# Kernel tuning notes

Hardware: AMD Instinct MI355X
Metric: run time of the kernel (lower is better)

## Reference

```python
import jax, jax.numpy as jnp
import numpy as np

N = 20000
E = 320000
D_IN = 1024
D_OUT = 1024


def setup_inputs() -> dict:
    key = jax.random.key(0)
    k1, k2, k3, k4 = jax.random.split(key, 4)
    x = jax.random.normal(k1, (N, D_IN), dtype=jnp.float32)
    edge_index = jax.random.randint(k2, (2, E), 0, N, dtype=jnp.int64)
    # nn.Linear params: W is [out, in], b is [out]
    W = jax.random.normal(k3, (D_OUT, D_IN), dtype=jnp.float32) * (1.0 / np.sqrt(D_IN))
    b = jax.random.normal(k4, (D_OUT,), dtype=jnp.float32) * 0.01
    return {"x": x, "edge_index": edge_index, "W": W, "b": b}


def reference(x, edge_index, W, b):
    num_nodes = x.shape[0]
    # add self-connections (same as addSelfConnect)
    self_idx = jnp.arange(num_nodes, dtype=edge_index.dtype)
    ei = jnp.concatenate([edge_index, jnp.stack([self_idx, self_idx], axis=0)], axis=1)
    row, col = ei[0], ei[1]
    # linear: h = x @ W^T + b  -> [N, D_OUT]
    h = jnp.einsum('nd,od->no', x, W) + b
    # degree computed from row indices only (matches calDegree(row, ...))
    deg = jnp.zeros((num_nodes,), dtype=h.dtype).at[row].add(1.0)
    deg_inv_sqrt = deg ** -0.5  # every node has a self-loop, so deg >= 1
    norm = deg_inv_sqrt[row] * deg_inv_sqrt[col]  # [E+N]
    # gather source features, scale per-edge, scatter-sum to destination nodes
    msg = norm[:, None] * h[col]  # [E+N, D_OUT]
    out = jax.ops.segment_sum(msg, row, num_segments=num_nodes)
    return out
```

## Files before the change

kernel.cpp:

```cpp
#include <hip/hip_runtime.h>
#include <hip/hip_bf16.h>
#include <stdint.h>
#include <stddef.h>


#define D_DIM 1024

typedef __bf16 bf16x8 __attribute__((ext_vector_type(8)));
typedef __bf16 bf16x4 __attribute__((ext_vector_type(4)));
typedef float  f32x4  __attribute__((ext_vector_type(4)));

#define GLOBAL_AS __attribute__((address_space(1)))
#define LDS_AS    __attribute__((address_space(3)))

static __device__ __forceinline__ void async_load16(const void* g, void* l) {
  __builtin_amdgcn_global_load_lds((GLOBAL_AS void*)(void*)g,
                                   (LDS_AS void*)l, 16, 0, 0);
}


__global__ void detect_kernel(const unsigned int* __restrict__ xw,
                              const unsigned int* __restrict__ ww,
                              const unsigned int* __restrict__ ew,
                              int* __restrict__ flags) {
  __shared__ int s[3];
  int t = threadIdx.x;
  if (t < 3) s[t] = 0;
  __syncthreads();
  int nx = 0, nw = 0, ze = 0;
  for (int i = t; i < 8192; i += 256) {
    if ((xw[i] & 0x7f80u) == 0x7f80u) nx++;
    if ((ww[i] & 0x7f80u) == 0x7f80u) nw++;
    if (ew[2 * i + 1] == 0u) ze++;
  }
  atomicAdd(&s[0], nx);
  atomicAdd(&s[1], nw);
  atomicAdd(&s[2], ze);
  __syncthreads();
  if (t == 0) {
    flags[0] = (s[0] >= 3) ? 1 : 0;
    flags[1] = (s[1] >= 3) ? 1 : 0;
    flags[2] = (s[2] >= 8000) ? 1 : 0;
  }
}


__global__ void zero_cnt_kernel(int* cnt, int n) {
  int i = blockIdx.x * blockDim.x + threadIdx.x;
  if (i < n) cnt[i] = 0;
}

__global__ void count_deg_kernel(const void* __restrict__ ei, int E,
                                 const int* __restrict__ flags,
                                 int* __restrict__ cnt) {
  int e = blockIdx.x * blockDim.x + threadIdx.x;
  if (e < E) {
    int r = flags[2] ? (int)((const long long*)ei)[e] : ((const int*)ei)[e];
    atomicAdd(&cnt[r], 1);
  }
}

__global__ void scan_kernel(const int* __restrict__ cnt, int n,
                            int* __restrict__ row_ptr, int* __restrict__ cursor,
                            float* __restrict__ dinv) {
  __shared__ int ssum[256];
  const int t = threadIdx.x;
  const int chunk = (n + 255) / 256;
  const int lo = t * chunk;
  const int hi = (lo + chunk < n) ? lo + chunk : n;
  int s = 0;
  for (int i = lo; i < hi; ++i) s += cnt[i];
  ssum[t] = s;
  __syncthreads();
  for (int off = 1; off < 256; off <<= 1) {
    int add = (t >= off) ? ssum[t - off] : 0;
    __syncthreads();
    ssum[t] += add;
    __syncthreads();
  }
  int run = ssum[t] - s;
  for (int i = lo; i < hi; ++i) {
    int v = cnt[i];
    row_ptr[i] = run;
    cursor[i]  = run;
    dinv[i] = rsqrtf((float)(v + 1));
    run += v;
  }
  if (t == 255) row_ptr[n] = ssum[255];
}

__global__ void scatter_kernel(const void* __restrict__ ei, int E,
                               const int* __restrict__ flags,
                               const float* __restrict__ dinv,
                               int* __restrict__ cursor,
                               int* __restrict__ cols_out,
                               float* __restrict__ wgt, int emit_w) {
  int e = blockIdx.x * blockDim.x + threadIdx.x;
  if (e < E) {
    int r, c;
    if (flags[2]) {
      const long long* p = (const long long*)ei;
      r = (int)p[e]; c = (int)p[e + E];
    } else {
      const int* p = (const int*)ei;
      r = p[e]; c = p[e + E];
    }
    int pos = atomicAdd(&cursor[r], 1);
    cols_out[pos] = c;
    if (emit_w) wgt[pos] = dinv[r] * dinv[c];
  }
}


__global__ void conv_w_kernel(const void* __restrict__ W,
                              const void* __restrict__ b,
                              const int* __restrict__ flags,
                              unsigned short* __restrict__ Wb,
                              float* __restrict__ biasf) {
  int i = blockIdx.x * blockDim.x + threadIdx.x;
  int wfp = flags[1];
  if (wfp) {
    __bf16 h = (__bf16)((const float*)W)[i];
    Wb[i] = *(unsigned short*)&h;
  } else {
    Wb[i] = ((const unsigned short*)W)[i];
  }
  if (i < D_DIM) {
    biasf[i] = wfp ? ((const float*)b)[i] : (float)((const __bf16*)b)[i];
  }
}


__global__ __launch_bounds__(256) void conv_x_kernel(
    const void* __restrict__ X, const int* __restrict__ flags,
    unsigned short* __restrict__ Xb, int total8) {
  int i = blockIdx.x * blockDim.x + threadIdx.x;
  if (i >= total8) return;
  if (!flags[0]) return;
  const float* p = (const float*)X + (size_t)i * 8;
  f32x4 v0 = *(const f32x4*)p;
  f32x4 v1 = *(const f32x4*)(p + 4);
  bf16x8 r;
  r[0] = (__bf16)v0[0]; r[1] = (__bf16)v0[1];
  r[2] = (__bf16)v0[2]; r[3] = (__bf16)v0[3];
  r[4] = (__bf16)v1[0]; r[5] = (__bf16)v1[1];
  r[6] = (__bf16)v1[2]; r[7] = (__bf16)v1[3];
  *(bf16x8*)(Xb + (size_t)i * 8) = r;
}


__global__ __launch_bounds__(256) void gemm_xw2_kernel(
    const void* __restrict__ Xv,
    const unsigned short* __restrict__ Xb,
    const unsigned short* __restrict__ Wb,
    const float* __restrict__ biasf,
    const int* __restrict__ flags,
    __hip_bfloat16* __restrict__ H,
    int M) {
  __shared__ unsigned short As[128 * 32];
  __shared__ unsigned short Bs[128 * 32];

  const int t    = threadIdx.x;
  const int lane = t & 63;
  const int wave = t >> 6;
  const int wm   = wave >> 1;
  const int wn   = wave & 1;

  const int nwg = gridDim.x;
  const int wg  = (blockIdx.x & 7) * (nwg >> 3) + (blockIdx.x >> 3);
  const int m0  = (wg >> 3) * 128;
  const int n0  = (wg & 7) * 128;

  const unsigned short* Asrc =
      flags[0] ? Xb : (const unsigned short*)Xv;

  f32x4 acc[4][4] = {};

  const int ra = t >> 2;
  const int kc = (t & 3) * 8;
  int gr0 = m0 + ra;       if (gr0 >= M) gr0 = M - 1;
  int gr1 = m0 + 64 + ra;  if (gr1 >= M) gr1 = M - 1;
  const int quad = lane >> 4;
  const int mrow = lane & 15;

  for (int k0 = 0; k0 < D_DIM; k0 += 32) {
    async_load16(Asrc + (size_t)gr0 * D_DIM + k0 + kc, &As[ra * 32 + kc]);
    async_load16(Asrc + (size_t)gr1 * D_DIM + k0 + kc, &As[(ra + 64) * 32 + kc]);
    async_load16(Wb + (size_t)(n0 + ra) * D_DIM + k0 + kc, &Bs[ra * 32 + kc]);
    async_load16(Wb + (size_t)(n0 + ra + 64) * D_DIM + k0 + kc,
                 &Bs[(ra + 64) * 32 + kc]);
    __syncthreads();

    bf16x8 a[4], b[4];
#pragma unroll
    for (int i = 0; i < 4; ++i)
      a[i] = *(const bf16x8*)&As[(wm * 64 + i * 16 + mrow) * 32 + quad * 8];
#pragma unroll
    for (int j = 0; j < 4; ++j)
      b[j] = *(const bf16x8*)&Bs[(wn * 64 + j * 16 + mrow) * 32 + quad * 8];
#pragma unroll
    for (int i = 0; i < 4; ++i)
#pragma unroll
      for (int j = 0; j < 4; ++j)
        acc[i][j] = __builtin_amdgcn_mfma_f32_16x16x32_bf16(a[i], b[j], acc[i][j], 0, 0, 0);
    __syncthreads();
  }

#pragma unroll
  for (int j = 0; j < 4; ++j) {
    int n = n0 + wn * 64 + j * 16 + mrow;
    float bn = biasf[n];
#pragma unroll
    for (int i = 0; i < 4; ++i) {
      int mb = m0 + wm * 64 + i * 16 + quad * 4;
#pragma unroll
      for (int rg = 0; rg < 4; ++rg) {
        int m = mb + rg;
        if (m < M) H[(size_t)m * D_DIM + n] = __float2bfloat16(acc[i][j][rg] + bn);
      }
    }
  }
}


__global__ __launch_bounds__(256) void gemm_xw_kernel(
    const void* __restrict__ Xv,
    const unsigned short* __restrict__ Wb,
    const float* __restrict__ biasf,
    const int* __restrict__ flags,
    __hip_bfloat16* __restrict__ H,
    int M) {
  __shared__ unsigned short As[128 * 32];
  __shared__ unsigned short Bs[128 * 32];

  const int t    = threadIdx.x;
  const int lane = t & 63;
  const int wave = t >> 6;
  const int wm   = wave >> 1;
  const int wn   = wave & 1;
  const int m0   = blockIdx.x * 128;
  const int n0   = blockIdx.y * 128;
  const int xfp  = flags[0];

  f32x4 acc[4][4] = {};

  const int ra = t >> 1;
  const int kh = (t & 1) * 16;
  const int rb = t >> 2;
  const int kc = (t & 3) * 8;
  const int quad = lane >> 4;
  const int mrow = lane & 15;

  for (int k0 = 0; k0 < D_DIM; k0 += 32) {
    async_load16(Wb + (size_t)(n0 + rb) * D_DIM + k0 + kc, &Bs[rb * 32 + kc]);
    async_load16(Wb + (size_t)(n0 + rb + 64) * D_DIM + k0 + kc,
                 &Bs[(rb + 64) * 32 + kc]);
    bf16x8 lo{}, hi{};
    int gm = m0 + ra;
    if (gm < M) {
      if (xfp) {
        const float* p = (const float*)Xv + (size_t)gm * D_DIM + k0 + kh;
        f32x4 v0 = *(const f32x4*)(p);
        f32x4 v1 = *(const f32x4*)(p + 4);
        f32x4 v2 = *(const f32x4*)(p + 8);
        f32x4 v3 = *(const f32x4*)(p + 12);
        lo[0] = (__bf16)v0[0]; lo[1] = (__bf16)v0[1];
        lo[2] = (__bf16)v0[2]; lo[3] = (__bf16)v0[3];
        lo[4] = (__bf16)v1[0]; lo[5] = (__bf16)v1[1];
        lo[6] = (__bf16)v1[2]; lo[7] = (__bf16)v1[3];
        hi[0] = (__bf16)v2[0]; hi[1] = (__bf16)v2[1];
        hi[2] = (__bf16)v2[2]; hi[3] = (__bf16)v2[3];
        hi[4] = (__bf16)v3[0]; hi[5] = (__bf16)v3[1];
        hi[6] = (__bf16)v3[2]; hi[7] = (__bf16)v3[3];
      } else {
        const unsigned short* p =
            (const unsigned short*)Xv + (size_t)gm * D_DIM + k0 + kh;
        lo = *(const bf16x8*)p;
        hi = *(const bf16x8*)(p + 8);
      }
    }
    *(bf16x8*)&As[ra * 32 + kh]     = lo;
    *(bf16x8*)&As[ra * 32 + kh + 8] = hi;
    __syncthreads();

    bf16x8 a[4], b[4];
#pragma unroll
    for (int i = 0; i < 4; ++i)
      a[i] = *(const bf16x8*)&As[(wm * 64 + i * 16 + mrow) * 32 + quad * 8];
#pragma unroll
    for (int j = 0; j < 4; ++j)
      b[j] = *(const bf16x8*)&Bs[(wn * 64 + j * 16 + mrow) * 32 + quad * 8];
#pragma unroll
    for (int i = 0; i < 4; ++i)
#pragma unroll
      for (int j = 0; j < 4; ++j)
        acc[i][j] = __builtin_amdgcn_mfma_f32_16x16x32_bf16(a[i], b[j], acc[i][j], 0, 0, 0);
    __syncthreads();
  }

#pragma unroll
  for (int j = 0; j < 4; ++j) {
    int n = n0 + wn * 64 + j * 16 + mrow;
    float bn = biasf[n];
#pragma unroll
    for (int i = 0; i < 4; ++i) {
      int mb = m0 + wm * 64 + i * 16 + quad * 4;
#pragma unroll
      for (int rg = 0; rg < 4; ++rg) {
        int m = mb + rg;
        if (m < M) H[(size_t)m * D_DIM + n] = __float2bfloat16(acc[i][j][rg] + bn);
      }
    }
  }
}


__global__ __launch_bounds__(256) void aggregate_h_kernel(
    const __hip_bfloat16* __restrict__ H,
    const int* __restrict__ row_ptr,
    const int* __restrict__ cols,
    const float* __restrict__ wgt,
    const float* __restrict__ dinv,
    const int* __restrict__ flags,
    void* __restrict__ outv, int M) {
  const int lane = threadIdx.x & 63;
  const int i = blockIdx.x * 4 + (threadIdx.x >> 6);
  if (i >= M) return;
  const int c0 = lane * 16;

  float a[16];
  {
    float di = dinv[i];
    float w = di * di;
    const __hip_bfloat16* p = H + (size_t)i * D_DIM + c0;
    bf16x8 v0 = *(const bf16x8*)p;
    bf16x8 v1 = *(const bf16x8*)(p + 8);
#pragma unroll
    for (int k = 0; k < 8; ++k) {
      a[k]     = w * (float)v0[k];
      a[8 + k] = w * (float)v1[k];
    }
  }
  const int e0 = row_ptr[i], e1 = row_ptr[i + 1];
  for (int e = e0; e < e1; ++e) {
    int c = cols[e];
    float w = wgt[e];
    const __hip_bfloat16* p = H + (size_t)c * D_DIM + c0;
    bf16x8 u0 = *(const bf16x8*)p;
    bf16x8 u1 = *(const bf16x8*)(p + 8);
#pragma unroll
    for (int k = 0; k < 8; ++k) {
      a[k]     += w * (float)u0[k];
      a[8 + k] += w * (float)u1[k];
    }
  }
  if (flags[0]) {
    float* o = (float*)outv + (size_t)i * D_DIM + c0;
#pragma unroll
    for (int q = 0; q < 4; ++q) {
      f32x4 r; r[0] = a[4*q]; r[1] = a[4*q+1]; r[2] = a[4*q+2]; r[3] = a[4*q+3];
      *(f32x4*)(o + 4 * q) = r;
    }
  } else {
    __hip_bfloat16* o = (__hip_bfloat16*)outv + (size_t)i * D_DIM + c0;
    bf16x8 r0, r1;
#pragma unroll
    for (int k = 0; k < 8; ++k) { r0[k] = (__bf16)a[k]; r1[k] = (__bf16)a[8+k]; }
    *(bf16x8*)o = r0;
    *(bf16x8*)(o + 8) = r1;
  }
}


__global__ __launch_bounds__(256) void aggregate_x_kernel(
    const void* __restrict__ X,
    const int* __restrict__ row_ptr,
    const int* __restrict__ cols,
    const float* __restrict__ dinv,
    const int* __restrict__ flags,
    float* __restrict__ rowsum,
    void* __restrict__ Y) {
  const int i  = blockIdx.x;
  const int c0 = threadIdx.x * 4;
  const float di = dinv[i];
  const int e0 = row_ptr[i], e1 = row_ptr[i + 1];
  float wsum = di * di;
  float a0, a1, a2, a3;

  if (flags[0]) {
    const float* Xf = (const float*)X;
    f32x4 v = *(const f32x4*)(Xf + (size_t)i * D_DIM + c0);
    a0 = wsum * v[0]; a1 = wsum * v[1]; a2 = wsum * v[2]; a3 = wsum * v[3];
    for (int e = e0; e < e1; ++e) {
      int c = cols[e];
      float w = di * dinv[c];
      wsum += w;
      f32x4 u = *(const f32x4*)(Xf + (size_t)c * D_DIM + c0);
      a0 += w * u[0]; a1 += w * u[1]; a2 += w * u[2]; a3 += w * u[3];
    }
    f32x4 r; r[0] = a0; r[1] = a1; r[2] = a2; r[3] = a3;
    *(f32x4*)((float*)Y + (size_t)i * D_DIM + c0) = r;
  } else {
    const __hip_bfloat16* Xb = (const __hip_bfloat16*)X;
    bf16x4 v = *(const bf16x4*)(Xb + (size_t)i * D_DIM + c0);
    a0 = wsum * (float)v[0]; a1 = wsum * (float)v[1];
    a2 = wsum * (float)v[2]; a3 = wsum * (float)v[3];
    for (int e = e0; e < e1; ++e) {
      int c = cols[e];
      float w = di * dinv[c];
      wsum += w;
      bf16x4 u = *(const bf16x4*)(Xb + (size_t)c * D_DIM + c0);
      a0 += w * (float)u[0]; a1 += w * (float)u[1];
      a2 += w * (float)u[2]; a3 += w * (float)u[3];
    }
    bf16x4 r;
    r[0] = (__bf16)a0; r[1] = (__bf16)a1; r[2] = (__bf16)a2; r[3] = (__bf16)a3;
    *(bf16x4*)((__hip_bfloat16*)Y + (size_t)i * D_DIM + c0) = r;
  }
  if (threadIdx.x == 0) rowsum[i] = wsum;
}

__global__ __launch_bounds__(256) void strip_gemm_kernel(
    const void* __restrict__ Yv,
    const unsigned short* __restrict__ Wb,
    const float* __restrict__ biasf,
    const float* __restrict__ rowsum,
    const int* __restrict__ flags,
    void* __restrict__ outv) {
  __shared__ unsigned short Ys[32 * 1024];

  const int t    = threadIdx.x;
  const int lane = t & 63;
  const int wave = t >> 6;
  const int m0   = blockIdx.x * 32;
  const int ofp  = flags[0];

  if (ofp) {
    const float* Yf = (const float*)Yv;
    for (int idx = t; idx < 32 * 128; idx += 256) {
      int r = idx >> 7, c = idx & 127;
      const float* p = Yf + (size_t)(m0 + r) * D_DIM + c * 8;
      f32x4 lo = *(const f32x4*)p;
      f32x4 hi = *(const f32x4*)(p + 4);
      bf16x8 v;
      v[0] = (__bf16)lo[0]; v[1] = (__bf16)lo[1];
      v[2] = (__bf16)lo[2]; v[3] = (__bf16)lo[3];
      v[4] = (__bf16)hi[0]; v[5] = (__bf16)hi[1];
      v[6] = (__bf16)hi[2]; v[7] = (__bf16)hi[3];
      int sc = c ^ (r & 15);
      *(bf16x8*)&Ys[r * 1024 + sc * 8] = v;
    }
  } else {
    const __hip_bfloat16* Yb = (const __hip_bfloat16*)Yv;
    for (int idx = t; idx < 32 * 128; idx += 256) {
      int r = idx >> 7, c = idx & 127;
      bf16x8 v = *(const bf16x8*)(Yb + (size_t)(m0 + r) * D_DIM + c * 8);
      int sc = c ^ (r & 15);
      *(bf16x8*)&Ys[r * 1024 + sc * 8] = v;
    }
  }
  __syncthreads();

  const int quad = lane >> 4;
  const int mrow = lane & 15;

  for (int nb = 0; nb < 4; ++nb) {
    f32x4 acc[2][4] = {};
    for (int k0 = 0; k0 < D_DIM; k0 += 32) {
      const int cbase = k0 >> 3;
      bf16x8 a[2], b[4];
#pragma unroll
      for (int i = 0; i < 2; ++i) {
        int m = i * 16 + mrow;
        int sc = (cbase + quad) ^ mrow;
        a[i] = *(const bf16x8*)&Ys[m * 1024 + sc * 8];
      }
#pragma unroll
      for (int j = 0; j < 4; ++j) {
        int n = wave * 256 + nb * 64 + j * 16 + mrow;
        b[j] = *(const bf16x8*)(Wb + (size_t)n * D_DIM + k0 + quad * 8);
      }
#pragma unroll
      for (int i = 0; i < 2; ++i)
#pragma unroll
        for (int j = 0; j < 4; ++j)
          acc[i][j] = __builtin_amdgcn_mfma_f32_16x16x32_bf16(a[i], b[j], acc[i][j], 0, 0, 0);
    }
#pragma unroll
    for (int j = 0; j < 4; ++j) {
      int n = wave * 256 + nb * 64 + j * 16 + mrow;
      float bn = biasf[n];
#pragma unroll
      for (int i = 0; i < 2; ++i) {
        int mb = m0 + i * 16 + quad * 4;
#pragma unroll
        for (int rg = 0; rg < 4; ++rg) {
          int m = mb + rg;
          float val = acc[i][j][rg] + rowsum[m] * bn;
          if (ofp) ((float*)outv)[(size_t)m * D_DIM + n] = val;
          else ((__hip_bfloat16*)outv)[(size_t)m * D_DIM + n] = __float2bfloat16(val);
        }
      }
    }
  }
}


extern "C" void kernel_launch(void* const* d_in, const int* in_sizes, int n_in,
                              void* d_out, int out_size, void* d_ws, size_t ws_size,
                              hipStream_t stream) {
  const void* x    = d_in[0];
  const void* ei   = d_in[1];
  const void* Wm   = d_in[2];
  const void* bias = d_in[3];

  const int E = in_sizes[1] / 2;
  const int M = in_sizes[0] / D_DIM;

  char* ws = (char*)d_ws;
  const size_t KB = 1024, MB = 1024 * 1024;

  const size_t szH = (size_t)M * D_DIM * 2;
  const size_t need_fast   = 6 * MB + szH + MB;
  const size_t need_faster = 6 * MB + 2 * szH + MB;

  if (ws_size >= need_fast) {
    int*   flags   = (int*)(ws);
    int*   cnt     = (int*)(ws + 4 * KB);
    int*   row_ptr = (int*)(ws + 128 * KB);
    int*   cursor  = (int*)(ws + 256 * KB);
    float* dinv    = (float*)(ws + 384 * KB);
    float* biasf   = (float*)(ws + 512 * KB);
    int*   cols    = (int*)(ws + 768 * KB);
    float* wgt     = (float*)(ws + 2 * MB);
    unsigned short* Wb = (unsigned short*)(ws + 4 * MB);
    __hip_bfloat16* H  = (__hip_bfloat16*)(ws + 6 * MB);
    unsigned short* Xb = (unsigned short*)(ws + 6 * MB + szH);

    detect_kernel<<<1, 256, 0, stream>>>((const unsigned int*)x,
                                         (const unsigned int*)Wm,
                                         (const unsigned int*)ei, (int*)flags);
    zero_cnt_kernel<<<(M + 255) / 256, 256, 0, stream>>>(cnt, M);
    count_deg_kernel<<<(E + 255) / 256, 256, 0, stream>>>(ei, E, flags, cnt);
    scan_kernel<<<1, 256, 0, stream>>>(cnt, M, row_ptr, cursor, dinv);
    scatter_kernel<<<(E + 255) / 256, 256, 0, stream>>>(ei, E, flags, dinv,
                                                        cursor, cols, wgt, 1);
    conv_w_kernel<<<(D_DIM * D_DIM) / 256, 256, 0, stream>>>(Wm, bias, flags,
                                                             Wb, biasf);
    const int mtiles = (M + 127) / 128;
    if (ws_size >= need_faster) {
      const int total8 = M * (D_DIM / 8);
      conv_x_kernel<<<(total8 + 255) / 256, 256, 0, stream>>>(x, flags, Xb,
                                                              total8);
      gemm_xw2_kernel<<<mtiles * 8, 256, 0, stream>>>(x, Xb, Wb, biasf, flags,
                                                      H, M);
    } else {
      dim3 ggrid(mtiles, D_DIM / 128);
      gemm_xw_kernel<<<ggrid, 256, 0, stream>>>(x, Wb, biasf, flags, H, M);
    }
    aggregate_h_kernel<<<(M + 3) / 4, 256, 0, stream>>>(H, row_ptr, cols, wgt,
                                                        dinv, flags, d_out, M);
  } else {
    int*   flags   = (int*)(ws);
    int*   cnt     = (int*)(ws + 4 * KB);
    int*   row_ptr = (int*)(ws + 128 * KB);
    int*   cursor  = (int*)(ws + 256 * KB);
    float* dinv    = (float*)(ws + 384 * KB);
    float* rowsum  = (float*)(ws + 512 * KB);
    float* biasf   = (float*)(ws + 640 * KB);
    int*   cols    = (int*)(ws + 768 * KB);
    unsigned short* Wb = (unsigned short*)(ws + 2 * MB);

    detect_kernel<<<1, 256, 0, stream>>>((const unsigned int*)x,
                                         (const unsigned int*)Wm,
                                         (const unsigned int*)ei, (int*)flags);
    zero_cnt_kernel<<<(M + 255) / 256, 256, 0, stream>>>(cnt, M);
    count_deg_kernel<<<(E + 255) / 256, 256, 0, stream>>>(ei, E, flags, cnt);
    scan_kernel<<<1, 256, 0, stream>>>(cnt, M, row_ptr, cursor, dinv);
    scatter_kernel<<<(E + 255) / 256, 256, 0, stream>>>(ei, E, flags, dinv,
                                                        cursor, cols, (float*)0, 0);
    conv_w_kernel<<<(D_DIM * D_DIM) / 256, 256, 0, stream>>>(Wm, bias, flags,
                                                             Wb, biasf);
    aggregate_x_kernel<<<M, 256, 0, stream>>>(x, row_ptr, cols, dinv, flags,
                                              rowsum, d_out);
    strip_gemm_kernel<<<M / 32, 256, 0, stream>>>(d_out, Wb, biasf, rowsum,
                                                  flags, d_out);
  }
}
```

Before: 428.3 us.

## Slab-tile aggregation over feature columns with padded H and packed edge metadata

The aggregation kernel now splits the 1024 feature columns into 16 slabs of 64 and assigns 8 threads per node per slab. Slab-major block ordering keeps the gathered working set of H small enough to stay cache-resident while all nodes are processed. H rows are padded to 1088 elements to avoid channel or bank aliasing. Column index and edge weight are packed into one 64-bit word, the edge loop is unrolled by four with FMAs, and outputs use nontemporal stores. The cost is 16 times more row_ptr and metadata reads, extra workspace for the padding, and a possible stride-related change in GEMM write efficiency.

```diff
diff --git a/kernel.cpp b/kernel.cpp
--- a/kernel.cpp
+++ b/kernel.cpp
@@ -5,6 +5,10 @@
 
 
 #define D_DIM 1024
+#define HP    1088
+#define HPB   2176u
+#define SLABW 64
+#define NSLAB (D_DIM / SLABW)
 
 typedef __bf16 bf16x8 __attribute__((ext_vector_type(8)));
 typedef __bf16 bf16x4 __attribute__((ext_vector_type(4)));
@@ -94,7 +98,7 @@
                                const float* __restrict__ dinv,
                                int* __restrict__ cursor,
                                int* __restrict__ cols_out,
-                               float* __restrict__ wgt, int emit_w) {
+                               long long* __restrict__ meta, int emit_w) {
   int e = blockIdx.x * blockDim.x + threadIdx.x;
   if (e < E) {
     int r, c;
@@ -106,8 +110,14 @@
       r = p[e]; c = p[e + E];
     }
     int pos = atomicAdd(&cursor[r], 1);
-    cols_out[pos] = c;
-    if (emit_w) wgt[pos] = dinv[r] * dinv[c];
+    if (emit_w) {
+      float w = dinv[r] * dinv[c];
+      unsigned long long mm =
+          ((unsigned long long)__float_as_uint(w) << 32) | (unsigned)c;
+      meta[pos] = (long long)mm;
+    } else {
+      cols_out[pos] = c;
+    }
   }
 }
 
@@ -216,7 +226,7 @@
 #pragma unroll
       for (int rg = 0; rg < 4; ++rg) {
         int m = mb + rg;
-        if (m < M) H[(size_t)m * D_DIM + n] = __float2bfloat16(acc[i][j][rg] + bn);
+        if (m < M) H[(size_t)m * HP + n] = __float2bfloat16(acc[i][j][rg] + bn);
       }
     }
   }
@@ -308,66 +318,88 @@
 #pragma unroll
       for (int rg = 0; rg < 4; ++rg) {
         int m = mb + rg;
-        if (m < M) H[(size_t)m * D_DIM + n] = __float2bfloat16(acc[i][j][rg] + bn);
+        if (m < M) H[(size_t)m * HP + n] = __float2bfloat16(acc[i][j][rg] + bn);
       }
     }
   }
 }
 
 
-__global__ __launch_bounds__(256) void aggregate_h_kernel(
+__global__ __launch_bounds__(256) void aggregate_h_slab_kernel(
     const __hip_bfloat16* __restrict__ H,
     const int* __restrict__ row_ptr,
-    const int* __restrict__ cols,
-    const float* __restrict__ wgt,
+    const long long* __restrict__ meta,
     const float* __restrict__ dinv,
     const int* __restrict__ flags,
-    void* __restrict__ outv, int M) {
-  const int lane = threadIdx.x & 63;
-  const int i = blockIdx.x * 4 + (threadIdx.x >> 6);
+    void* __restrict__ outv, int M, int nodeblks) {
+  const int slab = blockIdx.x / nodeblks;
+  const int nb   = blockIdx.x - slab * nodeblks;
+  const int t    = threadIdx.x;
+  const int i    = nb * 32 + (t >> 3);
   if (i >= M) return;
-  const int c0 = lane * 16;
-
-  float a[16];
+  const int l = t & 7;
+  const unsigned co = (unsigned)l * 16u;
+  const char* Hs = (const char*)H + (unsigned)slab * 128u;
+
+  float a[8];
   {
     float di = dinv[i];
     float w = di * di;
-    const __hip_bfloat16* p = H + (size_t)i * D_DIM + c0;
-    bf16x8 v0 = *(const bf16x8*)p;
-    bf16x8 v1 = *(const bf16x8*)(p + 8);
-#pragma unroll
-    for (int k = 0; k < 8; ++k) {
-      a[k]     = w * (float)v0[k];
-      a[8 + k] = w * (float)v1[k];
-    }
-  }
+    bf16x8 v = *(const bf16x8*)(Hs + (unsigned)i * HPB + co);
+#pragma unroll
+    for (int k = 0; k < 8; ++k) a[k] = w * (float)v[k];
+  }
+
   const int e0 = row_ptr[i], e1 = row_ptr[i + 1];
-  for (int e = e0; e < e1; ++e) {
-    int c = cols[e];
-    float w = wgt[e];
-    const __hip_bfloat16* p = H + (size_t)c * D_DIM + c0;
-    bf16x8 u0 = *(const bf16x8*)p;
-    bf16x8 u1 = *(const bf16x8*)(p + 8);
-#pragma unroll
-    for (int k = 0; k < 8; ++k) {
-      a[k]     += w * (float)u0[k];
-      a[8 + k] += w * (float)u1[k];
-    }
-  }
+  int e = e0;
+  for (; e + 4 <= e1; e += 4) {
+    long long m0 = meta[e];
+    long long m1 = meta[e + 1];
+    long long m2 = meta[e + 2];
+    long long m3 = meta[e + 3];
+    unsigned o0 = (unsigned)(m0 & 0xffffffffLL) * HPB + co;
+    unsigned o1 = (unsigned)(m1 & 0xffffffffLL) * HPB + co;
+    unsigned o2 = (unsigned)(m2 & 0xffffffffLL) * HPB + co;
+    unsigned o3 = (unsigned)(m3 & 0xffffffffLL) * HPB + co;
+    float w0 = __uint_as_float((unsigned)((unsigned long long)m0 >> 32));
+    float w1 = __uint_as_float((unsigned)((unsigned long long)m1 >> 32));
+    float w2 = __uint_as_float((unsigned)((unsigned long long)m2 >> 32));
+    float w3 = __uint_as_float((unsigned)((unsigned long long)m3 >> 32));
+    bf16x8 u0 = *(const bf16x8*)(Hs + o0);
+    bf16x8 u1 = *(const bf16x8*)(Hs + o1);
+    bf16x8 u2 = *(const bf16x8*)(Hs + o2);
+    bf16x8 u3 = *(const bf16x8*)(Hs + o3);
+#pragma unroll
+    for (int q = 0; q < 8; ++q) {
+      a[q] = fmaf(w0, (float)u0[q],
+             fmaf(w1, (float)u1[q],
+             fmaf(w2, (float)u2[q],
+             fmaf(w3, (float)u3[q], a[q]))));
+    }
+  }
+  for (; e < e1; ++e) {
+    long long m0 = meta[e];
+    unsigned o0 = (unsigned)(m0 & 0xffffffffLL) * HPB + co;
+    float w0 = __uint_as_float((unsigned)((unsigned long long)m0 >> 32));
+    bf16x8 u0 = *(const bf16x8*)(Hs + o0);
+#pragma unroll
+    for (int q = 0; q < 8; ++q) a[q] = fmaf(w0, (float)u0[q], a[q]);
+  }
+
   if (flags[0]) {
-    float* o = (float*)outv + (size_t)i * D_DIM + c0;
-#pragma unroll
-    for (int q = 0; q < 4; ++q) {
-      f32x4 r; r[0] = a[4*q]; r[1] = a[4*q+1]; r[2] = a[4*q+2]; r[3] = a[4*q+3];
-      *(f32x4*)(o + 4 * q) = r;
-    }
+    float* o = (float*)outv + (size_t)i * D_DIM + slab * SLABW + l * 8;
+    f32x4 r0, r1;
+    r0[0] = a[0]; r0[1] = a[1]; r0[2] = a[2]; r0[3] = a[3];
+    r1[0] = a[4]; r1[1] = a[5]; r1[2] = a[6]; r1[3] = a[7];
+    __builtin_nontemporal_store(r0, (f32x4*)o);
+    __builtin_nontemporal_store(r1, (f32x4*)(o + 4));
   } else {
-    __hip_bfloat16* o = (__hip_bfloat16*)outv + (size_t)i * D_DIM + c0;
-    bf16x8 r0, r1;
-#pragma unroll
-    for (int k = 0; k < 8; ++k) { r0[k] = (__bf16)a[k]; r1[k] = (__bf16)a[8+k]; }
-    *(bf16x8*)o = r0;
-    *(bf16x8*)(o + 8) = r1;
+    __hip_bfloat16* o =
+        (__hip_bfloat16*)outv + (size_t)i * D_DIM + slab * SLABW + l * 8;
+    bf16x8 r;
+#pragma unroll
+    for (int k = 0; k < 8; ++k) r[k] = (__bf16)a[k];
+    __builtin_nontemporal_store(*(f32x4*)&r, (f32x4*)o);
   }
 }
 
@@ -520,22 +552,34 @@
   char* ws = (char*)d_ws;
   const size_t KB = 1024, MB = 1024 * 1024;
 
-  const size_t szH = (size_t)M * D_DIM * 2;
-  const size_t need_fast   = 6 * MB + szH + MB;
-  const size_t need_faster = 6 * MB + 2 * szH + MB;
-
-  if (ws_size >= need_fast) {
-    int*   flags   = (int*)(ws);
-    int*   cnt     = (int*)(ws + 4 * KB);
-    int*   row_ptr = (int*)(ws + 128 * KB);
-    int*   cursor  = (int*)(ws + 256 * KB);
-    float* dinv    = (float*)(ws + 384 * KB);
-    float* biasf   = (float*)(ws + 512 * KB);
-    int*   cols    = (int*)(ws + 768 * KB);
-    float* wgt     = (float*)(ws + 2 * MB);
-    unsigned short* Wb = (unsigned short*)(ws + 4 * MB);
-    __hip_bfloat16* H  = (__hip_bfloat16*)(ws + 6 * MB);
-    unsigned short* Xb = (unsigned short*)(ws + 6 * MB + szH);
+  const size_t off_flags = 0;
+  const size_t off_cnt   = 4 * KB;
+  const size_t off_biasf = 96 * KB;
+  const size_t off_rowp  = 128 * KB;
+  const size_t off_curs  = off_rowp + 96 * KB;
+  const size_t off_dinv  = off_curs + 96 * KB;
+  const size_t off_meta  = off_dinv + 128 * KB;
+  size_t off_wb = off_meta + (size_t)E * 8;
+  off_wb = (off_wb + 255) & ~(size_t)255;
+  const size_t off_h  = off_wb + 2 * MB;
+  const size_t szHp   = (size_t)M * HP * 2;
+  const size_t off_xb = off_h + szHp;
+  const size_t szXb   = (size_t)M * D_DIM * 2;
+
+  const size_t need_fast   = off_h + szHp + 64 * KB;
+  const size_t need_faster = off_xb + szXb + 64 * KB;
+
+  if (ws_size >= need_fast && M > 256) {
+    int*   flags   = (int*)(ws + off_flags);
+    int*   cnt     = (int*)(ws + off_cnt);
+    float* biasf   = (float*)(ws + off_biasf);
+    int*   row_ptr = (int*)(ws + off_rowp);
+    int*   cursor  = (int*)(ws + off_curs);
+    float* dinv    = (float*)(ws + off_dinv);
+    long long* meta = (long long*)(ws + off_meta);
+    unsigned short* Wb = (unsigned short*)(ws + off_wb);
+    __hip_bfloat16* H  = (__hip_bfloat16*)(ws + off_h);
+    unsigned short* Xb = (unsigned short*)(ws + off_xb);
 
     detect_kernel<<<1, 256, 0, stream>>>((const unsigned int*)x,
                                          (const unsigned int*)Wm,
@@ -544,7 +588,7 @@
     count_deg_kernel<<<(E + 255) / 256, 256, 0, stream>>>(ei, E, flags, cnt);
     scan_kernel<<<1, 256, 0, stream>>>(cnt, M, row_ptr, cursor, dinv);
     scatter_kernel<<<(E + 255) / 256, 256, 0, stream>>>(ei, E, flags, dinv,
-                                                        cursor, cols, wgt, 1);
+                                                        cursor, (int*)0, meta, 1);
     conv_w_kernel<<<(D_DIM * D_DIM) / 256, 256, 0, stream>>>(Wm, bias, flags,
                                                              Wb, biasf);
     const int mtiles = (M + 127) / 128;
@@ -558,8 +602,9 @@
       dim3 ggrid(mtiles, D_DIM / 128);
       gemm_xw_kernel<<<ggrid, 256, 0, stream>>>(x, Wb, biasf, flags, H, M);
     }
-    aggregate_h_kernel<<<(M + 3) / 4, 256, 0, stream>>>(H, row_ptr, cols, wgt,
-                                                        dinv, flags, d_out, M);
+    const int nodeblks = (M + 31) / 32;
+    aggregate_h_slab_kernel<<<nodeblks * NSLAB, 256, 0, stream>>>(
+        H, row_ptr, meta, dinv, flags, d_out, M, nodeblks);
   } else {
     int*   flags   = (int*)(ws);
     int*   cnt     = (int*)(ws + 4 * KB);
@@ -578,7 +623,7 @@
     count_deg_kernel<<<(E + 255) / 256, 256, 0, stream>>>(ei, E, flags, cnt);
     scan_kernel<<<1, 256, 0, stream>>>(cnt, M, row_ptr, cursor, dinv);
     scatter_kernel<<<(E + 255) / 256, 256, 0, stream>>>(ei, E, flags, dinv,
-                                                        cursor, cols, (float*)0, 0);
+                                                        cursor, cols, (long long*)0, 0);
     conv_w_kernel<<<(D_DIM * D_DIM) / 256, 256, 0, stream>>>(Wm, bias, flags,
                                                              Wb, biasf);
     aggregate_x_kernel<<<M, 256, 0, stream>>>(x, row_ptr, cols, dinv, flags,
```

Measured after the change: 410.8 us. 4.1% less time.
